# Kernel optimization log

Measured on AMD Instinct MI355X. Metric: run time of the kernel, lower is better.

The kernel has to match this reference:

```python
import jax, jax.numpy as jnp
import numpy as np
from jax import lax

T = 8192
OBS = 512
HID = 2048
NOBJ = 8


def setup_inputs() -> dict:
    key = jax.random.key(0)
    ks = jax.random.split(key, 9)
    s_in = 1.0 / np.sqrt(OBS)
    s_hid = 1.0 / np.sqrt(HID)
    return {
        "x": jax.random.normal(ks[0], (T, OBS), dtype=jnp.float32),
        "W_in": jax.random.normal(ks[1], (HID, OBS), dtype=jnp.float32) * s_in,
        "W_B": jax.random.normal(ks[2], (HID, OBS), dtype=jnp.float32) * s_in,
        "W_C": jax.random.normal(ks[3], (HID, OBS), dtype=jnp.float32) * s_in,
        "W_delta": jax.random.normal(ks[4], (HID, OBS), dtype=jnp.float32) * s_in,
        "A_log": jax.random.normal(ks[5], (HID,), dtype=jnp.float32),
        "W_out": jax.random.normal(ks[6], (NOBJ, HID), dtype=jnp.float32) * s_hid,
        "b_out": jnp.zeros((NOBJ,), dtype=jnp.float32),
        "W_skip": jax.random.normal(ks[7], (NOBJ, OBS), dtype=jnp.float32) * s_in,
    }


def reference(x, W_in, W_B, W_C, W_delta, A_log, W_out, b_out, W_skip):
    # Input-dependent SSM parameters (4 GEMMs, [T, HID] each)
    x_state = x @ W_in.T
    B = x @ W_B.T
    C = x @ W_C.T
    delta = jax.nn.sigmoid(x @ W_delta.T)
    A = -jnp.exp(A_log)                      # [HID]

    A_bar = jnp.exp(delta * A)               # [T, HID], per-step decay
    Bx = B * x_state                         # [T, HID], per-step input

    def step(h, inp):
        a, bx = inp
        h = a * h + bx
        return h, h

    h0 = jnp.zeros((HID,), dtype=x.dtype)
    _, h_seq = lax.scan(step, h0, (A_bar, Bx))  # [T, HID]

    y = C * h_seq
    out = y @ W_out.T + b_out + x @ W_skip.T    # [T, NOBJ]
    return out
```

## Files before the change

### kernel.cpp

```cpp
#include <hip/hip_runtime.h>
#include <hip/hip_bf16.h>
#include <cstdint>

#define TT   8192
#define KOBS 512
#define HID  2048
#define NOBJ 8
#define NCH  128
#define CT   64

typedef unsigned short u16;
typedef uint32_t u32;
typedef short bf16x8 __attribute__((ext_vector_type(8)));
typedef float f32x4  __attribute__((ext_vector_type(4)));
typedef unsigned short u16x4 __attribute__((ext_vector_type(4)));

static __device__ __forceinline__ float bf2f(u16 u) {
    union { uint32_t i; float f; } v;
    v.i = ((uint32_t)u) << 16;
    return v.f;
}
static __device__ __forceinline__ u16 f2bf(float f) {
    union { float f; uint32_t i; } v;
    v.f = f;
    uint32_t lsb = (v.i >> 16) & 1u;
    uint32_t r = v.i + 0x7fffu + lsb;
    return (u16)(r >> 16);
}

static __device__ __forceinline__ void async_ld16(const u16* g, u16* l) {
    __builtin_amdgcn_global_load_lds(
        (const __attribute__((address_space(1))) uint32_t*)g,
        (__attribute__((address_space(3))) uint32_t*)l,
        16, 0, 0);
}

__global__ void prep_w(const float* __restrict__ Win,
                       const float* __restrict__ WB,
                       const float* __restrict__ WC,
                       const float* __restrict__ Wd,
                       const float* __restrict__ A_log,
                       u16* __restrict__ W_bf,
                       float* __restrict__ A_e)
{
    const int tid0   = blockIdx.x * blockDim.x + threadIdx.x;
    const int stride = gridDim.x * blockDim.x;

    for (int i = tid0; i < 4 * HID * KOBS / 8; i += stride) {
        int n  = i >> 6;
        int k8 = (i & 63) * 8;
        int h  = n >> 2;
        int w  = n & 3;
        const float* src = (w == 0) ? Win : (w == 1) ? WB : (w == 2) ? WC : Wd;
        const float4* s4 = (const float4*)(src + (size_t)h * KOBS + k8);
        float4 a = s4[0], b = s4[1];
        u16x4 o1 = { f2bf(a.x), f2bf(a.y), f2bf(a.z), f2bf(a.w) };
        u16x4 o2 = { f2bf(b.x), f2bf(b.y), f2bf(b.z), f2bf(b.w) };
        *(u16x4*)&W_bf[(size_t)i * 8]     = o1;
        *(u16x4*)&W_bf[(size_t)i * 8 + 4] = o2;
    }

    if (tid0 < HID)
        A_e[tid0] = -__expf(A_log[tid0]) * 1.44269504f;
}

__launch_bounds__(256)
__global__ void prep_x_out(const float* __restrict__ x,
                           const float* __restrict__ b_out,
                           const float* __restrict__ W_skip,
                           float* __restrict__ out,
                           u16* __restrict__ x_bf)
{
    const int wave = threadIdx.x >> 6;
    const int lane = threadIdx.x & 63;
    const int t0 = (blockIdx.x * 4 + wave) * 4;

    float acc[4][NOBJ];
#pragma unroll
    for (int tt = 0; tt < 4; tt++)
#pragma unroll
        for (int o = 0; o < NOBJ; o++) acc[tt][o] = 0.f;

#pragma unroll
    for (int i = 0; i < 2; i++) {
        const int kv = (i * 64 + lane) * 4;
        float4 w[NOBJ];
#pragma unroll
        for (int o = 0; o < NOBJ; o++)
            w[o] = *(const float4*)(W_skip + (size_t)o * KOBS + kv);
#pragma unroll
        for (int tt = 0; tt < 4; tt++) {
            const size_t off = (size_t)(t0 + tt) * KOBS + kv;
            float4 xv = *(const float4*)(x + off);
            u16x4 xb = { f2bf(xv.x), f2bf(xv.y), f2bf(xv.z), f2bf(xv.w) };
            *(u16x4*)&x_bf[off] = xb;
#pragma unroll
            for (int o = 0; o < NOBJ; o++)
                acc[tt][o] += xv.x * w[o].x + xv.y * w[o].y +
                              xv.z * w[o].z + xv.w * w[o].w;
        }
    }
#pragma unroll
    for (int s = 32; s > 0; s >>= 1)
#pragma unroll
        for (int tt = 0; tt < 4; tt++)
#pragma unroll
            for (int o = 0; o < NOBJ; o++)
                acc[tt][o] += __shfl_xor(acc[tt][o], s, 64);
    if (lane == 0) {
#pragma unroll
        for (int tt = 0; tt < 4; tt++)
#pragma unroll
            for (int o = 0; o < NOBJ; o++)
                out[(size_t)(t0 + tt) * NOBJ + o] = acc[tt][o] + b_out[o];
    }
}

__launch_bounds__(256)
__global__ void gemm_fused(const u16* __restrict__ x_bf,
                           const u16* __restrict__ W_bf,
                           const float* __restrict__ A_e,
                           u16* __restrict__ G,
                           float* __restrict__ P,
                           float* __restrict__ S)
{
    __shared__ __align__(16) u16 smem[128 * 37 * 4];
    __shared__ float Ps[256], Ss[256];
    u16* a_s = smem;
    u16* b_s = smem + 4096;

    const int tid  = threadIdx.x;
    const int bm   = blockIdx.x & 63;
    const int bn   = blockIdx.x >> 6;
    const int m0t  = bm * 128;
    const int n0   = bn * 128;
    const int lane = tid & 63;
    const int wave = tid >> 6;
    const int wn   = (wave & 1) * 64;
    const int wt   = (wave >> 1) * 64;
    const int fr   = lane & 15;
    const int fq   = lane >> 4;

    f32x4 acc[4][4];
#pragma unroll
    for (int i = 0; i < 4; i++)
#pragma unroll
        for (int j = 0; j < 4; j++) {
            f32x4 z = {0.f, 0.f, 0.f, 0.f};
            acc[i][j] = z;
        }

    const int srow = tid >> 2;
    const int scg  = (tid & 3) ^ ((srow >> 1) & 3);
    const u16* gA0 = x_bf + (size_t)(m0t + srow) * KOBS + scg * 8;
    const u16* gA1 = gA0 + (size_t)64 * KOBS;
    const u16* gB0 = W_bf + (size_t)(n0 + srow) * KOBS + scg * 8;
    const u16* gB1 = gB0 + (size_t)64 * KOBS;
    u16* lA0 = &a_s[tid * 8];
    u16* lA1 = &a_s[2048 + tid * 8];
    u16* lB0 = &b_s[tid * 8];
    u16* lB1 = &b_s[2048 + tid * 8];

    const int pcg = fq ^ ((fr >> 1) & 3);

    for (int kb = 0; kb < KOBS; kb += 32) {
        async_ld16(gA0 + kb, lA0);
        async_ld16(gA1 + kb, lA1);
        async_ld16(gB0 + kb, lB0);
        async_ld16(gB1 + kb, lB1);
        __syncthreads();

        bf16x8 af[4], bfx[4];
#pragma unroll
        for (int i = 0; i < 4; i++)
            af[i] = *(const bf16x8*)&b_s[(wn + i * 16 + fr) * 32 + pcg * 8];
#pragma unroll
        for (int j = 0; j < 4; j++)
            bfx[j] = *(const bf16x8*)&a_s[(wt + j * 16 + fr) * 32 + pcg * 8];

#pragma unroll
        for (int i = 0; i < 4; i++)
#pragma unroll
            for (int j = 0; j < 4; j++)
                acc[i][j] = __builtin_amdgcn_mfma_f32_16x16x32_bf16(
                    af[i], bfx[j], acc[i][j], 0, 0, 0);
        __syncthreads();
    }

    const int hq = wn >> 2;
#pragma unroll
    for (int i = 0; i < 4; i++) {
        const int hl = hq + i * 4 + fq;
        const float ae = A_e[bn * 32 + hl];
#pragma unroll
        for (int j = 0; j < 4; j++) {
            const int tl = wt + j * 16 + fr;
            f32x4 v = acc[i][j];
            float sig = 1.0f / (1.0f + __expf(-v[3]));
            u32 lo = (u32)f2bf(v[0] * v[1]) | ((u32)f2bf(v[2]) << 16);
            u32 hi = (u32)f2bf(sig * ae);
            *(uint2*)&smem[(tl * 37 + hl) * 4] = make_uint2(lo, hi);
        }
    }
    __syncthreads();

#pragma unroll
    for (int it = 0; it < 8; it++) {
        const int g   = it * 256 + tid;
        const int row = g >> 4;
        const int c2  = g & 15;
        uint2 lo = *(const uint2*)&smem[(row * 37 + c2 * 2) * 4];
        uint2 hi = *(const uint2*)&smem[(row * 37 + c2 * 2 + 1) * 4];
        uint4 v = make_uint4(lo.x, lo.y, hi.x, hi.y);
        *(uint4*)(G + ((size_t)(m0t + row) * HID + bn * 32 + c2 * 2) * 4) = v;
    }

    {
        const int hi  = tid & 31;
        const int seg = tid >> 5;
        float p = 1.f, s = 0.f;
        const int tbase = seg * 16;
#pragma unroll
        for (int t = 0; t < 16; t++) {
            uint2 w = *(const uint2*)&smem[((tbase + t) * 37 + hi) * 4];
            float a  = exp2f(bf2f((u16)(w.y & 0xffff)));
            float bx = bf2f((u16)(w.x & 0xffff));
            s = fmaf(a, s, bx);
            p *= a;
        }
        Ps[seg * 32 + hi] = p;
        Ss[seg * 32 + hi] = s;
        __syncthreads();
        if (tid < 64) {
            const int half = tid >> 5, h2 = tid & 31;
            float pt = 1.f, st = 0.f;
#pragma unroll
            for (int sg = 0; sg < 4; sg++) {
                float ps = Ps[(half * 4 + sg) * 32 + h2];
                float ss = Ss[(half * 4 + sg) * 32 + h2];
                st = fmaf(ps, st, ss);
                pt *= ps;
            }
            P[(size_t)(bm * 2 + half) * HID + bn * 32 + h2] = pt;
            S[(size_t)(bm * 2 + half) * HID + bn * 32 + h2] = st;
        }
    }
}

__global__ void scan_combine(const float* __restrict__ P,
                             const float* __restrict__ S,
                             float* __restrict__ H0)
{
    const int h = blockIdx.x * 256 + threadIdx.x;
    float hrun = 0.f;
#pragma unroll 8
    for (int c = 0; c < NCH; c++) {
        H0[c * HID + h] = hrun;
        hrun = fmaf(P[c * HID + h], hrun, S[c * HID + h]);
    }
}

__launch_bounds__(256)
__global__ void scan_out(const u16* __restrict__ G,
                         const float* __restrict__ H0,
                         const float* __restrict__ W_out,
                         float* __restrict__ out)
{
    __shared__ __align__(16) u16 ybuf[CT * 256];
    __shared__ __align__(16) u16 wst[8 * 264];
    const int tid  = threadIdx.x;
    const int c    = blockIdx.x >> 3;
    const int hg   = blockIdx.x & 7;
    const int lane = tid & 63;
    const int wave = tid >> 6;
    const int fr   = lane & 15;
    const int fq   = lane >> 4;

#pragma unroll
    for (int o = 0; o < 8; o++)
        wst[o * 264 + tid] = f2bf(W_out[(size_t)o * HID + hg * 256 + tid]);

    const int h = hg * 256 + tid;
    float hrun = H0[c * HID + h];
    size_t base = (size_t)c * CT * HID + h;
    const int g  = tid >> 3;
    const int lo = tid & 7;
    for (int tb = 0; tb < CT; tb += 8) {
        uint2 wv[8];
#pragma unroll
        for (int q = 0; q < 8; q++)
            wv[q] = *(const uint2*)&G[(base + (size_t)q * HID) * 4];
#pragma unroll
        for (int q = 0; q < 8; q++) {
            float bx = bf2f((u16)(wv[q].x & 0xffff));
            float cc = bf2f((u16)(wv[q].x >> 16));
            float a  = exp2f(bf2f((u16)(wv[q].y & 0xffff)));
            hrun = fmaf(a, hrun, bx);
            const int t = tb + q;
            ybuf[t * 256 + (((g ^ (t & 7)) << 3) | lo)] = f2bf(cc * hrun);
        }
        base += (size_t)8 * HID;
    }
    __syncthreads();

    bf16x8 bw[8];
#pragma unroll
    for (int ks = 0; ks < 8; ks++) {
        bf16x8 w = {0, 0, 0, 0, 0, 0, 0, 0};
        if (fr < 8)
            w = *(const bf16x8*)&wst[fr * 264 + ks * 32 + fq * 8];
        bw[ks] = w;
    }

    {
        const int tb = wave * 16;
        const int t  = tb + fr;
        f32x4 acc2 = {0.f, 0.f, 0.f, 0.f};
#pragma unroll
        for (int ks = 0; ks < 8; ks++) {
            const int gg = ks * 4 + fq;
            bf16x8 yv = *(const bf16x8*)
                &ybuf[t * 256 + ((gg ^ (fr & 7)) << 3)];
            acc2 = __builtin_amdgcn_mfma_f32_16x16x32_bf16(bw[ks], yv, acc2,
                                                           0, 0, 0);
        }
        if (fq < 2) {
            const int tg = c * CT + t;
#pragma unroll
            for (int reg = 0; reg < 4; reg++)
                atomicAdd(&out[(size_t)tg * NOBJ + 4 * fq + reg], acc2[reg]);
        }
    }
}

extern "C" void kernel_launch(void* const* d_in, const int* in_sizes, int n_in,
                              void* d_out, int out_size, void* d_ws, size_t ws_size,
                              hipStream_t stream)
{
    const float* x      = (const float*)d_in[0];
    const float* Win    = (const float*)d_in[1];
    const float* WB     = (const float*)d_in[2];
    const float* WC     = (const float*)d_in[3];
    const float* Wd     = (const float*)d_in[4];
    const float* A_log  = (const float*)d_in[5];
    const float* W_out  = (const float*)d_in[6];
    const float* b_out  = (const float*)d_in[7];
    const float* W_skip = (const float*)d_in[8];
    float* out = (float*)d_out;

    char* ws = (char*)d_ws;
    size_t off = 0;
    auto alloc = [&](size_t bytes) -> void* {
        void* p = (void*)(ws + off);
        off += (bytes + 255) & ~(size_t)255;
        return p;
    };

    u16*   x_bf = (u16*)  alloc((size_t)TT * KOBS * 2);
    u16*   W_bf = (u16*)  alloc((size_t)4 * HID * KOBS * 2);
    float* A_e  = (float*)alloc((size_t)HID * 4);
    u16*   G    = (u16*)  alloc((size_t)TT * HID * 8);
    float* P    = (float*)alloc((size_t)NCH * HID * 4);
    float* S    = (float*)alloc((size_t)NCH * HID * 4);
    float* H0   = (float*)alloc((size_t)NCH * HID * 4);
    (void)ws_size; (void)in_sizes; (void)n_in; (void)out_size;

    prep_w<<<2048, 256, 0, stream>>>(Win, WB, WC, Wd, A_log, W_bf, A_e);
    prep_x_out<<<512, 256, 0, stream>>>(x, b_out, W_skip, out, x_bf);
    gemm_fused<<<4096, 256, 0, stream>>>(x_bf, W_bf, A_e, G, P, S);
    scan_combine<<<8, 256, 0, stream>>>(P, S, H0);
    scan_out<<<1024, 256, 0, stream>>>(G, H0, W_out, out);
}
```

Measured before the change: 229.6 us.

## Compute local scan in GEMM epilogue and emit affine y coefficients

The GEMM epilogue now runs the full within-tile scan. It writes two bf16 arrays, YB = C*h_local and YC = C*cumprod(a), instead of an 8-byte packed G tensor. The final kernel then reconstructs y = YB + YC*h0 with a single fused multiply-add, dropping the serial 64-step scan over G. This halves the intermediate global traffic and removes the sequential dependency from the last kernel, at the cost of extra epilogue work and an extra rounding of YC*h0 in bf16. The chunk count also drops to 64 chunks of 128 steps, which matches the GEMM tile.

Result: faster. 217.3 us (-5.3%).

```diff
diff --git a/kernel.cpp b/kernel.cpp
--- a/kernel.cpp
+++ b/kernel.cpp
@@ -6,8 +6,8 @@
 #define KOBS 512
 #define HID  2048
 #define NOBJ 8
-#define NCH  128
-#define CT   64
+#define NCH  64
+#define CT   128
 
 typedef unsigned short u16;
 typedef uint32_t u32;
@@ -120,11 +120,12 @@
 __global__ void gemm_fused(const u16* __restrict__ x_bf,
                            const u16* __restrict__ W_bf,
                            const float* __restrict__ A_e,
-                           u16* __restrict__ G,
+                           u16* __restrict__ YB,
+                           u16* __restrict__ YC,
                            float* __restrict__ P,
                            float* __restrict__ S)
 {
-    __shared__ __align__(16) u16 smem[128 * 37 * 4];
+    __shared__ __align__(16) u16 smem[3 * 128 * 40];
     __shared__ float Ps[256], Ss[256];
     u16* a_s = smem;
     u16* b_s = smem + 4096;
@@ -197,53 +198,75 @@
             const int tl = wt + j * 16 + fr;
             f32x4 v = acc[i][j];
             float sig = 1.0f / (1.0f + __expf(-v[3]));
-            u32 lo = (u32)f2bf(v[0] * v[1]) | ((u32)f2bf(v[2]) << 16);
-            u32 hi = (u32)f2bf(sig * ae);
-            *(uint2*)&smem[(tl * 37 + hl) * 4] = make_uint2(lo, hi);
-        }
-    }
-    __syncthreads();
-
-#pragma unroll
-    for (int it = 0; it < 8; it++) {
-        const int g   = it * 256 + tid;
-        const int row = g >> 4;
-        const int c2  = g & 15;
-        uint2 lo = *(const uint2*)&smem[(row * 37 + c2 * 2) * 4];
-        uint2 hi = *(const uint2*)&smem[(row * 37 + c2 * 2 + 1) * 4];
-        uint4 v = make_uint4(lo.x, lo.y, hi.x, hi.y);
-        *(uint4*)(G + ((size_t)(m0t + row) * HID + bn * 32 + c2 * 2) * 4) = v;
-    }
-
+            smem[(0 * 128 + tl) * 40 + hl] = f2bf(v[0] * v[1]);
+            smem[(1 * 128 + tl) * 40 + hl] = f2bf(v[2]);
+            smem[(2 * 128 + tl) * 40 + hl] = f2bf(sig * ae);
+        }
+    }
+    __syncthreads();
+
+    const int hi  = tid & 31;
+    const int seg = tid >> 5;
     {
-        const int hi  = tid & 31;
-        const int seg = tid >> 5;
         float p = 1.f, s = 0.f;
         const int tbase = seg * 16;
 #pragma unroll
         for (int t = 0; t < 16; t++) {
-            uint2 w = *(const uint2*)&smem[((tbase + t) * 37 + hi) * 4];
-            float a  = exp2f(bf2f((u16)(w.y & 0xffff)));
-            float bx = bf2f((u16)(w.x & 0xffff));
+            float a  = exp2f(bf2f(smem[(2 * 128 + tbase + t) * 40 + hi]));
+            float bx = bf2f(smem[(0 * 128 + tbase + t) * 40 + hi]);
             s = fmaf(a, s, bx);
             p *= a;
         }
         Ps[seg * 32 + hi] = p;
         Ss[seg * 32 + hi] = s;
-        __syncthreads();
-        if (tid < 64) {
-            const int half = tid >> 5, h2 = tid & 31;
-            float pt = 1.f, st = 0.f;
-#pragma unroll
-            for (int sg = 0; sg < 4; sg++) {
-                float ps = Ps[(half * 4 + sg) * 32 + h2];
-                float ss = Ss[(half * 4 + sg) * 32 + h2];
-                st = fmaf(ps, st, ss);
-                pt *= ps;
-            }
-            P[(size_t)(bm * 2 + half) * HID + bn * 32 + h2] = pt;
-            S[(size_t)(bm * 2 + half) * HID + bn * 32 + h2] = st;
-        }
+    }
+    __syncthreads();
+
+    if (tid < 32) {
+        float rr = 1.f, sr = 0.f;
+#pragma unroll
+        for (int sg = 0; sg < 8; sg++) {
+            float ps = Ps[sg * 32 + tid], ss = Ss[sg * 32 + tid];
+            Ps[sg * 32 + tid] = rr;
+            Ss[sg * 32 + tid] = sr;
+            sr = fmaf(ps, sr, ss);
+            rr *= ps;
+        }
+        P[(size_t)bm * HID + bn * 32 + tid] = rr;
+        S[(size_t)bm * HID + bn * 32 + tid] = sr;
+    }
+    __syncthreads();
+
+    {
+        const float Rp = Ps[seg * 32 + hi];
+        const float Sp = Ss[seg * 32 + hi];
+        float r = 1.f, s = 0.f;
+        const int tbase = seg * 16;
+#pragma unroll
+        for (int t = 0; t < 16; t++) {
+            const int row = tbase + t;
+            float a  = exp2f(bf2f(smem[(2 * 128 + row) * 40 + hi]));
+            float bx = bf2f(smem[(0 * 128 + row) * 40 + hi]);
+            float cc = bf2f(smem[(1 * 128 + row) * 40 + hi]);
+            s = fmaf(a, s, bx);
+            r *= a;
+            float hl = fmaf(r, Sp, s);
+            smem[(0 * 128 + row) * 40 + hi] = f2bf(cc * hl);
+            smem[(2 * 128 + row) * 40 + hi] = f2bf(cc * r * Rp);
+        }
+    }
+    __syncthreads();
+
+#pragma unroll
+    for (int it = 0; it < 4; it++) {
+        const int g = it * 64 + (tid >> 2);
+        const int a = g >> 7;
+        const int t = g & 127;
+        const int c = tid & 3;
+        uint4 vd = *(const uint4*)&smem[((a * 2) * 128 + t) * 40 + c * 8];
+        u16* dst = (a == 0 ? YB : YC) +
+                   (size_t)(m0t + t) * HID + bn * 32 + c * 8;
+        *(uint4*)dst = vd;
     }
 }
 
@@ -261,45 +284,49 @@
 }
 
 __launch_bounds__(256)
-__global__ void scan_out(const u16* __restrict__ G,
-                         const float* __restrict__ H0,
-                         const float* __restrict__ W_out,
-                         float* __restrict__ out)
-{
-    __shared__ __align__(16) u16 ybuf[CT * 256];
+__global__ void final_out(const u16* __restrict__ YB,
+                          const u16* __restrict__ YC,
+                          const float* __restrict__ H0,
+                          const float* __restrict__ W_out,
+                          float* __restrict__ out)
+{
+    __shared__ __align__(16) u16 ybuf[64 * 256];
     __shared__ __align__(16) u16 wst[8 * 264];
+    __shared__ float h0s[256];
     const int tid  = threadIdx.x;
-    const int c    = blockIdx.x >> 3;
+    const int tc   = blockIdx.x >> 3;
     const int hg   = blockIdx.x & 7;
     const int lane = tid & 63;
     const int wave = tid >> 6;
     const int fr   = lane & 15;
     const int fq   = lane >> 4;
+    const int t0   = tc * 64;
 
 #pragma unroll
     for (int o = 0; o < 8; o++)
         wst[o * 264 + tid] = f2bf(W_out[(size_t)o * HID + hg * 256 + tid]);
-
-    const int h = hg * 256 + tid;
-    float hrun = H0[c * HID + h];
-    size_t base = (size_t)c * CT * HID + h;
-    const int g  = tid >> 3;
-    const int lo = tid & 7;
-    for (int tb = 0; tb < CT; tb += 8) {
-        uint2 wv[8];
-#pragma unroll
-        for (int q = 0; q < 8; q++)
-            wv[q] = *(const uint2*)&G[(base + (size_t)q * HID) * 4];
-#pragma unroll
-        for (int q = 0; q < 8; q++) {
-            float bx = bf2f((u16)(wv[q].x & 0xffff));
-            float cc = bf2f((u16)(wv[q].x >> 16));
-            float a  = exp2f(bf2f((u16)(wv[q].y & 0xffff)));
-            hrun = fmaf(a, hrun, bx);
-            const int t = tb + q;
-            ybuf[t * 256 + (((g ^ (t & 7)) << 3) | lo)] = f2bf(cc * hrun);
-        }
-        base += (size_t)8 * HID;
+    h0s[tid] = H0[(size_t)(tc >> 1) * HID + hg * 256 + tid];
+    __syncthreads();
+
+    const int g   = tid & 31;
+    const int tb0 = tid >> 5;
+    float4 h0a = *(const float4*)&h0s[g * 8];
+    float4 h0b = *(const float4*)&h0s[g * 8 + 4];
+    const float h0r[8] = { h0a.x, h0a.y, h0a.z, h0a.w,
+                           h0b.x, h0b.y, h0b.z, h0b.w };
+#pragma unroll
+    for (int k = 0; k < 8; k++) {
+        const int t = tb0 + k * 8;
+        const size_t off = (size_t)(t0 + t) * HID + hg * 256 + g * 8;
+        bf16x8 yb = *(const bf16x8*)(YB + off);
+        bf16x8 yc = *(const bf16x8*)(YC + off);
+        bf16x8 yv;
+#pragma unroll
+        for (int e = 0; e < 8; e++) {
+            float y = fmaf(bf2f((u16)yc[e]), h0r[e], bf2f((u16)yb[e]));
+            yv[e] = (short)f2bf(y);
+        }
+        *(bf16x8*)&ybuf[t * 256 + ((g ^ (t & 7)) << 3)] = yv;
     }
     __syncthreads();
 
@@ -313,8 +340,7 @@
     }
 
     {
-        const int tb = wave * 16;
-        const int t  = tb + fr;
+        const int t = wave * 16 + fr;
         f32x4 acc2 = {0.f, 0.f, 0.f, 0.f};
 #pragma unroll
         for (int ks = 0; ks < 8; ks++) {
@@ -325,7 +351,7 @@
                                                            0, 0, 0);
         }
         if (fq < 2) {
-            const int tg = c * CT + t;
+            const int tg = t0 + t;
 #pragma unroll
             for (int reg = 0; reg < 4; reg++)
                 atomicAdd(&out[(size_t)tg * NOBJ + 4 * fq + reg], acc2[reg]);
@@ -359,7 +385,8 @@
     u16*   x_bf = (u16*)  alloc((size_t)TT * KOBS * 2);
     u16*   W_bf = (u16*)  alloc((size_t)4 * HID * KOBS * 2);
     float* A_e  = (float*)alloc((size_t)HID * 4);
-    u16*   G    = (u16*)  alloc((size_t)TT * HID * 8);
+    u16*   YB   = (u16*)  alloc((size_t)TT * HID * 2);
+    u16*   YC   = (u16*)  alloc((size_t)TT * HID * 2);
     float* P    = (float*)alloc((size_t)NCH * HID * 4);
     float* S    = (float*)alloc((size_t)NCH * HID * 4);
     float* H0   = (float*)alloc((size_t)NCH * HID * 4);
@@ -367,7 +394,7 @@
 
     prep_w<<<2048, 256, 0, stream>>>(Win, WB, WC, Wd, A_log, W_bf, A_e);
     prep_x_out<<<512, 256, 0, stream>>>(x, b_out, W_skip, out, x_bf);
-    gemm_fused<<<4096, 256, 0, stream>>>(x_bf, W_bf, A_e, G, P, S);
+    gemm_fused<<<4096, 256, 0, stream>>>(x_bf, W_bf, A_e, YB, YC, P, S);
     scan_combine<<<8, 256, 0, stream>>>(P, S, H0);
-    scan_out<<<1024, 256, 0, stream>>>(G, H0, W_out, out);
-}
+    final_out<<<1024, 256, 0, stream>>>(YB, YC, H0, W_out, out);
+}
```
